# Performance work log

Hardware: AMD Instinct MI355X
Metric: run time of the kernel (lower is better)

## Reference

```python
import jax, jax.numpy as jnp
import numpy as np

D = 1024       # d_model
H = 16         # nhead
HD = D // H    # head_dim = 64
FF = 4096      # dim_feedforward
EPS = 1e-5


def layer_norm(x, gamma, beta, eps=EPS):
    mu = jnp.mean(x, axis=-1, keepdims=True)
    var = jnp.var(x, axis=-1, keepdims=True)
    return (x - mu) * jax.lax.rsqrt(var + eps) * gamma + beta


def setup_inputs() -> dict:
    key = jax.random.key(0)
    ks = jax.random.split(key, 12)
    rn = lambda k, shape, s=0.02: (jax.random.normal(k, shape, jnp.float32) * s)
    return {
        "src": jax.random.normal(ks[0], (4, 2048, D), jnp.float32),
        "Wqkv": rn(ks[1], (D, 3 * D)),          # qkv_proj weight (bias=False), stored (in,out)
        "Wout": rn(ks[2], (D, D)),              # out_proj weight (bias=False)
        "W1": rn(ks[3], (D, FF)),               # linear1
        "b1": jnp.zeros((FF,), jnp.float32),
        "W2": rn(ks[4], (FF, D)),               # linear2
        "b2": jnp.zeros((D,), jnp.float32),
        "g1": jnp.ones((D,), jnp.float32),      # norm1 weight
        "be1": jnp.zeros((D,), jnp.float32),    # norm1 bias
        "g2": jnp.ones((D,), jnp.float32),      # norm2 weight
        "be2": jnp.zeros((D,), jnp.float32),    # norm2 bias
    }


def reference(src, Wqkv, Wout, W1, b1, W2, b2, g1, be1, g2, be2):
    B, S, _ = src.shape
    # --- self attention (naive/MATH-backend SDPA, post-norm, eval: dropout=0) ---
    qkv = src @ Wqkv                                  # [B,S,3D]
    qkv = qkv.reshape(B, S, 3, H, HD)
    q = qkv[:, :, 0].transpose(0, 2, 1, 3)            # [B,H,S,HD]
    k = qkv[:, :, 1].transpose(0, 2, 1, 3)
    v = qkv[:, :, 2].transpose(0, 2, 1, 3)
    scores = jnp.einsum("bhqd,bhkd->bhqk", q, k) / np.float32(np.sqrt(HD))  # [B,H,S,S]
    attn = jax.nn.softmax(scores, axis=-1)
    ctx = jnp.einsum("bhqk,bhkd->bhqd", attn, v)      # [B,H,S,HD]
    ctx = ctx.transpose(0, 2, 1, 3).reshape(B, S, D)  # [B,S,D]
    attn_out = ctx @ Wout
    # residual + norm1
    x = layer_norm(src + attn_out, g1, be1)
    # --- FFN ---
    ff = jax.nn.relu(x @ W1 + b1) @ W2 + b2
    # residual + norm2
    return layer_norm(x + ff, g2, be2)
```

## Files before the change

kernel.cpp:

```cpp
#include <hip/hip_runtime.h>
#include <hip/hip_bf16.h>


typedef __attribute__((ext_vector_type(8))) short          short8;
typedef __attribute__((ext_vector_type(8))) unsigned short ushort8;
typedef __attribute__((ext_vector_type(4))) float          f32x4;
typedef __attribute__((ext_vector_type(2))) unsigned int   uivec2;

__device__ __forceinline__ unsigned short f2bf(float f) {
    union { float f; unsigned int u; } v; v.f = f;
    unsigned int u = v.u;
    unsigned int r = (u + 0x7fffu + ((u >> 16) & 1u)) >> 16;
    return (unsigned short)r;
}

__device__ __forceinline__ float bf2f(unsigned short u) {
    union { unsigned int u; float f; } v; v.u = ((unsigned int)u) << 16;
    return v.f;
}

__device__ __forceinline__ unsigned int pack_bf16_trunc(float lo, float hi) {
    union { float f; unsigned int u; } a, b; a.f = lo; b.f = hi;
    return __builtin_amdgcn_perm(b.u, a.u, 0x07060302u);
}

__device__ __forceinline__ void async_load16(const void* g, void* l) {
    __builtin_amdgcn_global_load_lds(
        (const __attribute__((address_space(1))) void*)(unsigned long long)g,
        (__attribute__((address_space(3))) void*)(unsigned long long)l,
        16, 0, 0);
}

__global__ __launch_bounds__(256) void cast_bf16_kernel(
    const float* __restrict__ x, unsigned short* __restrict__ y) {
    size_t i = ((size_t)blockIdx.x * 256 + threadIdx.x) * 4;
    float4 v = *(const float4*)(x + i);
    ushort4 o; o.x = f2bf(v.x); o.y = f2bf(v.y); o.z = f2bf(v.z); o.w = f2bf(v.w);
    *(ushort4*)(y + i) = o;
}

__global__ __launch_bounds__(256) void transpose_cast_kernel(
    const float* __restrict__ W, unsigned short* __restrict__ Wt, int K, int N) {
    __shared__ float tile[32][33];
    int n0 = blockIdx.x * 32, k0 = blockIdx.y * 32;
    int tx = threadIdx.x & 31, ty = threadIdx.x >> 5;
#pragma unroll
    for (int i = 0; i < 32; i += 8)
        tile[ty + i][tx] = W[(size_t)(k0 + ty + i) * N + n0 + tx];
    __syncthreads();
#pragma unroll
    for (int i = 0; i < 32; i += 8)
        Wt[(size_t)(n0 + ty + i) * K + k0 + tx] = f2bf(tile[tx][ty + i]);
}

template <int MODE>
__global__ __launch_bounds__(256) void gemm_bf16_kernel(
    const unsigned short* __restrict__ A, const unsigned short* __restrict__ Bt,
    int M, int N, int K, int Kstride,
    float* __restrict__ outF, unsigned short* __restrict__ outB,
    const float* __restrict__ bias,
    const float* __restrict__ resF, const unsigned short* __restrict__ resB,
    unsigned short* __restrict__ vtB) {
    __shared__ unsigned short As[2][128 * 32];
    __shared__ unsigned short Bs[2][128 * 32];

    const int t = threadIdx.x;
    const int m0 = blockIdx.x * 128, n0 = blockIdx.y * 128;
    const int koff = blockIdx.z * K;
    const int wid = t >> 6, lane = t & 63;
    const int wm = wid >> 1, wn = wid & 1;
    const int lr = lane & 15, quad = lane >> 4;

    const int srow = lane >> 2;
    const int sch  = ((lane & 3) ^ (srow & 3)) * 8;
    const unsigned short* Ag =
        A  + (size_t)(m0 + wid * 32 + srow) * Kstride + koff + sch;
    const unsigned short* Bg =
        Bt + (size_t)(n0 + wid * 32 + srow) * Kstride + koff + sch;
    const int wofs = (wid * 32) * 32;
    const size_t rstep = (size_t)16 * Kstride;

    const int axs = ((quad ^ (lr & 3))) * 8;
    f32x4 acc[4][4] = {};

    const int nK = K >> 5;
    async_load16(Ag,         &As[0][wofs]);
    async_load16(Ag + rstep, &As[0][wofs + 16 * 32]);
    async_load16(Bg,         &Bs[0][wofs]);
    async_load16(Bg + rstep, &Bs[0][wofs + 16 * 32]);

    for (int kt = 0; kt < nK; kt++) {
        const int cur = kt & 1, nxt = cur ^ 1;
        __syncthreads();
        if (kt + 1 < nK) {
            const int k1 = (kt + 1) * 32;
            async_load16(Ag + k1,         &As[nxt][wofs]);
            async_load16(Ag + k1 + rstep, &As[nxt][wofs + 16 * 32]);
            async_load16(Bg + k1,         &Bs[nxt][wofs]);
            async_load16(Bg + k1 + rstep, &Bs[nxt][wofs + 16 * 32]);
        }

        short8 af[4], bfr[4];
#pragma unroll
        for (int i = 0; i < 4; i++) {
            af[i]  = *(const short8*)&As[cur][(wm * 64 + i * 16 + lr) * 32 + axs];
            bfr[i] = *(const short8*)&Bs[cur][(wn * 64 + i * 16 + lr) * 32 + axs];
        }
#pragma unroll
        for (int mi = 0; mi < 4; mi++)
#pragma unroll
            for (int ni = 0; ni < 4; ni++)
                acc[mi][ni] = __builtin_amdgcn_mfma_f32_16x16x32_bf16(
                    af[mi], bfr[ni], acc[mi][ni], 0, 0, 0);
    }

#pragma unroll
    for (int mi = 0; mi < 4; mi++)
#pragma unroll
        for (int ni = 0; ni < 4; ni++) {
            const int col  = n0 + wn * 64 + ni * 16 + lr;
            const int row0 = m0 + wm * 64 + mi * 16 + quad * 4;
#pragma unroll
            for (int r = 0; r < 4; r++) {
                size_t idx = (size_t)(row0 + r) * N + col;
                float v = acc[mi][ni][r];
                if (MODE == 0) {
                    outB[idx] = f2bf(v);
                } else if (MODE == 1) {
                    outF[idx] = v + resF[idx];
                }
            }
        }
}

#define GBAR() do { __builtin_amdgcn_sched_barrier(0); \
                    __builtin_amdgcn_s_barrier();      \
                    __builtin_amdgcn_sched_barrier(0); } while (0)

template <int MODE>
__global__ __launch_bounds__(512, 2) void gemm256_bf16_kernel(
    const unsigned short* __restrict__ A, const unsigned short* __restrict__ Bt,
    int M, int N, int K, int Kstride,
    float* __restrict__ outF, unsigned short* __restrict__ outB,
    const float* __restrict__ bias,
    const float* __restrict__ resF, const unsigned short* __restrict__ resB,
    unsigned short* __restrict__ vtB) {
    __shared__ unsigned short Alds[4][256 * 32];
    __shared__ unsigned short Blds[4][256 * 32];

    const int t = threadIdx.x;
    const int wid = t >> 6, lane = t & 63;
    const int wm = wid >> 2, wn = wid & 3;
    const int lr = lane & 15, quad = lane >> 4;
    const int m0 = blockIdx.x * 256, n0 = blockIdx.y * 256;
    const int koff = blockIdx.z * K;

    const int srow = wid * 32 + (lane >> 2);
    const int sch  = ((lane & 3) ^ (srow & 3)) * 8;
    const unsigned short* Ag = A  + (size_t)(m0 + srow) * Kstride + koff + sch;
    const unsigned short* Bg = Bt + (size_t)(n0 + srow) * Kstride + koff + sch;
    const size_t rstep = (size_t)16 * Kstride;
    unsigned short* AdstW = &Alds[0][(wid * 32) * 32];
    unsigned short* BdstW = &Blds[0][(wid * 32) * 32];

    const int axs = (quad ^ (lr & 3)) * 8;

    f32x4 acc[8][4] = {};
    short8 bfr[4];

    const int T = K >> 6;
    const int Tm2 = T - 2, Tm3 = T - 3;

#define STAGE_A(GP) do { int s_ = (GP) & 3;                                   \
        const unsigned short* g_ = Ag + (GP) * 32;                            \
        async_load16(g_,         AdstW + s_ * 256 * 32);                      \
        async_load16(g_ + rstep, AdstW + s_ * 256 * 32 + 16 * 32); } while (0)
#define STAGE_B(GP) do { int s_ = (GP) & 3;                                   \
        const unsigned short* g_ = Bg + (GP) * 32;                            \
        async_load16(g_,         BdstW + s_ * 256 * 32);                      \
        async_load16(g_ + rstep, BdstW + s_ * 256 * 32 + 16 * 32); } while (0)

    STAGE_A(0); STAGE_B(0);
    STAGE_A(1); STAGE_B(1);
    STAGE_A(2); STAGE_B(2);
    asm volatile("s_waitcnt vmcnt(4)" ::: "memory");
    GBAR();

#define GPHASE(SLOT, MB, LOADB)                                               \
    {                                                                         \
        short8 af_[4];                                                        \
        _Pragma("unroll")                                                     \
        for (int i_ = 0; i_ < 4; i_++)                                        \
            af_[i_] = *(const short8*)                                        \
                &Alds[SLOT][(wm * 128 + ((MB) + i_) * 16 + lr) * 32 + axs];   \
        if (LOADB) {                                                          \
            _Pragma("unroll")                                                 \
            for (int i_ = 0; i_ < 4; i_++)                                    \
                bfr[i_] = *(const short8*)                                    \
                    &Blds[SLOT][(wn * 64 + i_ * 16 + lr) * 32 + axs];         \
        }

#define GPHASE_END(MB)                                                        \
        GBAR();                                                               \
        asm volatile("s_waitcnt lgkmcnt(0)" ::: "memory");                    \
        __builtin_amdgcn_sched_barrier(0);                                    \
        __builtin_amdgcn_s_setprio(1);                                        \
        _Pragma("unroll")                                                     \
        for (int mi_ = 0; mi_ < 4; mi_++)                                     \
            _Pragma("unroll")                                                 \
            for (int ni_ = 0; ni_ < 4; ni_++)                                 \
                acc[(MB) + mi_][ni_] = __builtin_amdgcn_mfma_f32_16x16x32_bf16( \
                    af_[mi_], bfr[ni_], acc[(MB) + mi_][ni_], 0, 0, 0);       \
        __builtin_amdgcn_s_setprio(0);                                        \
        GBAR();                                                               \
    }

    for (int t2 = 0; t2 < T; t2++) {
        const int s0 = (2 * t2) & 3, s1 = (2 * t2 + 1) & 3;
        const int gA = 2 * t2 + 3, gB = 2 * t2 + 4;

        GPHASE(s0, 0, 1)
            if (t2 <= Tm2) STAGE_A(gA);
        GPHASE_END(0)
        GPHASE(s0, 4, 0)
            if (t2 <= Tm2) STAGE_B(gA);
        GPHASE_END(4)
        GPHASE(s1, 0, 1)
            if (t2 <= Tm3) STAGE_A(gB);
        GPHASE_END(0)
        GPHASE(s1, 4, 0)
            if (t2 <= Tm3) STAGE_B(gB);
            if (t2 == Tm2) {
                asm volatile("s_waitcnt vmcnt(0)" ::: "memory");
            } else if (t2 < Tm2) {
                asm volatile("s_waitcnt vmcnt(4)" ::: "memory");
            }
        GPHASE_END(4)
    }

#undef GPHASE
#undef GPHASE_END
#undef STAGE_A
#undef STAGE_B

    const float QSC = 0.18033688011112042f;
    float* pOut = (MODE == 5) ? outF + (size_t)blockIdx.z * M * N : outF;
#pragma unroll
    for (int mi = 0; mi < 8; mi++)
#pragma unroll
        for (int ni = 0; ni < 4; ni++) {
            const int col  = n0 + wn * 64 + ni * 16 + lr;
            const int row0 = m0 + wm * 128 + mi * 16 + quad * 4;
            if (MODE == 4 && col >= 2048) {
                int bb = row0 >> 11, ss = row0 & 2047, c = col - 2048;
                ushort4 ov;
                ov.x = f2bf(acc[mi][ni][0]); ov.y = f2bf(acc[mi][ni][1]);
                ov.z = f2bf(acc[mi][ni][2]); ov.w = f2bf(acc[mi][ni][3]);
                *(ushort4*)&vtB[((size_t)bb * 1024 + c) * 2048 + ss] = ov;
            } else {
#pragma unroll
                for (int r = 0; r < 4; r++) {
                    size_t idx = (size_t)(row0 + r) * N + col;
                    float v = acc[mi][ni][r];
                    if (MODE == 4) {
                        outB[idx] = f2bf(col < 1024 ? v * QSC : v);
                    } else if (MODE == 2) {
                        v += bias[col];
                        outB[idx] = f2bf(v > 0.f ? v : 0.f);
                    } else if (MODE == 5) {
                        pOut[idx] = v;
                    }
                }
            }
        }
}

__global__ __launch_bounds__(256) void attention_kernel(
    const unsigned short* __restrict__ qkv, const unsigned short* __restrict__ Vt,
    unsigned short* __restrict__ ctx) {
    __shared__ unsigned short Kbuf[2][64 * 64];
    __shared__ unsigned short Vbuf[2][64 * 64];

    const int qt = blockIdx.x, h = blockIdx.y, b = blockIdx.z;
    const int t = threadIdx.x, wid = t >> 6, lane = t & 63;
    const int lr = lane & 15, quad = lane >> 4;
    const int q0 = qt * 64 + wid * 16;

    size_t qbase = ((size_t)(b * 2048 + q0 + lr)) * 3072 + h * 64;
    short8 qf0 = *(const short8*)(qkv + qbase + quad * 8);
    short8 qf1 = *(const short8*)(qkv + qbase + 32 + quad * 8);

    const int srow = wid * 8 + (lane >> 3);
    const int sch  = ((lane & 7) ^ (srow & 7)) * 8;
    const unsigned short* Kg =
        qkv + (size_t)b * 2048 * 3072 + 1024 + h * 64 + (size_t)srow * 3072 + sch;
    const unsigned short* Vg =
        Vt + ((size_t)b * 1024 + h * 64 + srow) * 2048 + sch;
    unsigned short* KsB = (unsigned short*)&Kbuf[0][(wid * 8) * 64];
    unsigned short* VsB = (unsigned short*)&Vbuf[0][(wid * 8) * 64];
    const int bufstep = 64 * 64;

    short8 ones;
#pragma unroll
    for (int i = 0; i < 8; i++) ones[i] = (short)0x3F80;

    f32x4 o[4] = {};
    f32x4 lacc = {};

#pragma unroll
    for (int half = 0; half < 2; half++) {
        async_load16(Kg + (size_t)(half * 32) * 3072, KsB + half * 32 * 64);
        async_load16(Vg + (size_t)(half * 32) * 2048, VsB + half * 32 * 64);
    }

    const int swz = lr & 7;

    for (int kt = 0; kt < 32; kt++) {
        const int cur = kt & 1, nxt = cur ^ 1;
        __syncthreads();
        if (kt + 1 < 32) {
#pragma unroll
            for (int half = 0; half < 2; half++) {
                async_load16(Kg + (size_t)((kt + 1) * 64 + half * 32) * 3072,
                             KsB + nxt * bufstep + half * 32 * 64);
                async_load16(Vg + (size_t)(half * 32) * 2048 + (kt + 1) * 64,
                             VsB + nxt * bufstep + half * 32 * 64);
            }
        }

        const unsigned short* Kc = &Kbuf[cur][0];
        const unsigned short* Vc = &Vbuf[cur][0];

        f32x4 s[4] = {};
#pragma unroll
        for (int nt = 0; nt < 4; nt++) {
            const unsigned short* krow = Kc + (nt * 16 + lr) * 64;
            short8 kf0 = *(const short8*)(krow + (quad ^ swz) * 8);
            short8 kf1 = *(const short8*)(krow + ((quad + 4) ^ swz) * 8);
            s[nt] = __builtin_amdgcn_mfma_f32_16x16x32_bf16(kf0, qf0, s[nt], 0, 0, 0);
            s[nt] = __builtin_amdgcn_mfma_f32_16x16x32_bf16(kf1, qf1, s[nt], 0, 0, 0);
        }

        unsigned int aw[4], bw[4];
#pragma unroll
        for (int nt = 0; nt < 4; nt++) {
            float p0 = __builtin_amdgcn_exp2f(s[nt][0]);
            float p1 = __builtin_amdgcn_exp2f(s[nt][1]);
            float p2 = __builtin_amdgcn_exp2f(s[nt][2]);
            float p3 = __builtin_amdgcn_exp2f(s[nt][3]);
            aw[nt] = pack_bf16_trunc(p0, p1);
            bw[nt] = pack_bf16_trunc(p2, p3);
        }

        uivec2 rA = __builtin_amdgcn_permlane32_swap(aw[0], aw[1], false, false);
        uivec2 sA = __builtin_amdgcn_permlane32_swap(aw[2], aw[3], false, false);
        uivec2 rB = __builtin_amdgcn_permlane32_swap(bw[0], bw[1], false, false);
        uivec2 sB = __builtin_amdgcn_permlane32_swap(bw[2], bw[3], false, false);
        uivec2 tA = __builtin_amdgcn_permlane16_swap(rA.x, rA.y, false, false);
        uivec2 uA = __builtin_amdgcn_permlane16_swap(sA.x, sA.y, false, false);
        uivec2 tB = __builtin_amdgcn_permlane16_swap(rB.x, rB.y, false, false);
        uivec2 uB = __builtin_amdgcn_permlane16_swap(sB.x, sB.y, false, false);

        union { unsigned int w[4]; short8 v; } P0, P1;
        P0.w[0] = tA.x; P0.w[1] = tB.x; P0.w[2] = tA.y; P0.w[3] = tB.y;
        P1.w[0] = uA.x; P1.w[1] = uB.x; P1.w[2] = uA.y; P1.w[3] = uB.y;
        short8 pf0 = P0.v;
        short8 pf1 = P1.v;

#pragma unroll
        for (int nt = 0; nt < 4; nt++) {
            const unsigned short* vrow = Vc + (nt * 16 + lr) * 64;
            short8 vf0 = *(const short8*)(vrow + (quad ^ swz) * 8);
            short8 vf1 = *(const short8*)(vrow + ((quad + 4) ^ swz) * 8);
            o[nt] = __builtin_amdgcn_mfma_f32_16x16x32_bf16(pf0, vf0, o[nt], 0, 0, 0);
            o[nt] = __builtin_amdgcn_mfma_f32_16x16x32_bf16(pf1, vf1, o[nt], 0, 0, 0);
        }
        lacc = __builtin_amdgcn_mfma_f32_16x16x32_bf16(pf0, ones, lacc, 0, 0, 0);
        lacc = __builtin_amdgcn_mfma_f32_16x16x32_bf16(pf1, ones, lacc, 0, 0, 0);
    }

#pragma unroll
    for (int r = 0; r < 4; r++) {
        float li = 1.f / lacc[r];
        int q = qt * 64 + wid * 16 + quad * 4 + r;
#pragma unroll
        for (int nt = 0; nt < 4; nt++)
            ctx[((size_t)(b * 2048 + q)) * 1024 + h * 64 + nt * 16 + lr] =
                f2bf(o[nt][r] * li);
    }
}

template <int OUTMODE>
__global__ __launch_bounds__(256) void layernorm_kernel(
    const float* __restrict__ x, const float* __restrict__ g,
    const float* __restrict__ be, float* __restrict__ yF,
    unsigned short* __restrict__ yB) {
    const int row = blockIdx.x, t = threadIdx.x;
    const float* xr = x + (size_t)row * 1024;
    float4 v = *(const float4*)(xr + t * 4);
    float s  = v.x + v.y + v.z + v.w;
    float sq = v.x * v.x + v.y * v.y + v.z * v.z + v.w * v.w;
#pragma unroll
    for (int d = 1; d < 64; d <<= 1) {
        s  += __shfl_xor(s, d, 64);
        sq += __shfl_xor(sq, d, 64);
    }
    __shared__ float sh[8];
    int wid = t >> 6, lane = t & 63;
    if (lane == 0) { sh[wid] = s; sh[4 + wid] = sq; }
    __syncthreads();
    s  = sh[0] + sh[1] + sh[2] + sh[3];
    sq = sh[4] + sh[5] + sh[6] + sh[7];
    float mu  = s * (1.f / 1024.f);
    float var = sq * (1.f / 1024.f) - mu * mu;
    float rstd = rsqrtf(var + 1e-5f);
    float4 gv = *(const float4*)(g + t * 4);
    float4 bv = *(const float4*)(be + t * 4);
    float4 y;
    y.x = (v.x - mu) * rstd * gv.x + bv.x;
    y.y = (v.y - mu) * rstd * gv.y + bv.y;
    y.z = (v.z - mu) * rstd * gv.z + bv.z;
    y.w = (v.w - mu) * rstd * gv.w + bv.w;
    if (OUTMODE == 0) {
        *(float4*)(yF + (size_t)row * 1024 + t * 4) = y;
    } else {
        ushort4 o;
        o.x = f2bf(y.x); o.y = f2bf(y.y); o.z = f2bf(y.z); o.w = f2bf(y.w);
        *(ushort4*)(yB + (size_t)row * 1024 + t * 4) = o;
    }
}

__global__ __launch_bounds__(256) void layernorm_sum2_kernel(
    const float* __restrict__ p0, const float* __restrict__ p1,
    const float* __restrict__ bias, const unsigned short* __restrict__ res,
    const float* __restrict__ g, const float* __restrict__ be,
    float* __restrict__ out) {
    const int row = blockIdx.x, t = threadIdx.x;
    const size_t base = (size_t)row * 1024 + t * 4;
    float4 a = *(const float4*)(p0 + base);
    float4 b = *(const float4*)(p1 + base);
    float4 bi = *(const float4*)(bias + t * 4);
    ushort4 rb = *(const ushort4*)(res + base);
    float4 v;
    v.x = a.x + b.x + bi.x + bf2f(rb.x);
    v.y = a.y + b.y + bi.y + bf2f(rb.y);
    v.z = a.z + b.z + bi.z + bf2f(rb.z);
    v.w = a.w + b.w + bi.w + bf2f(rb.w);
    float s  = v.x + v.y + v.z + v.w;
    float sq = v.x * v.x + v.y * v.y + v.z * v.z + v.w * v.w;
#pragma unroll
    for (int d = 1; d < 64; d <<= 1) {
        s  += __shfl_xor(s, d, 64);
        sq += __shfl_xor(sq, d, 64);
    }
    __shared__ float sh[8];
    int wid = t >> 6, lane = t & 63;
    if (lane == 0) { sh[wid] = s; sh[4 + wid] = sq; }
    __syncthreads();
    s  = sh[0] + sh[1] + sh[2] + sh[3];
    sq = sh[4] + sh[5] + sh[6] + sh[7];
    float mu  = s * (1.f / 1024.f);
    float var = sq * (1.f / 1024.f) - mu * mu;
    float rstd = rsqrtf(var + 1e-5f);
    float4 gv = *(const float4*)(g + t * 4);
    float4 bv = *(const float4*)(be + t * 4);
    float4 y;
    y.x = (v.x - mu) * rstd * gv.x + bv.x;
    y.y = (v.y - mu) * rstd * gv.y + bv.y;
    y.z = (v.z - mu) * rstd * gv.z + bv.z;
    y.w = (v.w - mu) * rstd * gv.w + bv.w;
    *(float4*)(out + base) = y;
}

extern "C" void kernel_launch(void* const* d_in, const int* in_sizes, int n_in,
                              void* d_out, int out_size, void* d_ws, size_t ws_size,
                              hipStream_t stream) {
    const float* src  = (const float*)d_in[0];
    const float* Wqkv = (const float*)d_in[1];
    const float* Wout = (const float*)d_in[2];
    const float* W1   = (const float*)d_in[3];
    const float* b1   = (const float*)d_in[4];
    const float* W2   = (const float*)d_in[5];
    const float* b2   = (const float*)d_in[6];
    const float* g1   = (const float*)d_in[7];
    const float* be1  = (const float*)d_in[8];
    const float* g2   = (const float*)d_in[9];
    const float* be2  = (const float*)d_in[10];
    float* out = (float*)d_out;

    const size_t NT = 8192;
    char* ws = (char*)d_ws;
    unsigned short* src_bf = (unsigned short*)ws; ws += NT * 1024 * 2;
    unsigned short* Wqkv_t = (unsigned short*)ws; ws += (size_t)3072 * 1024 * 2;
    unsigned short* Wout_t = (unsigned short*)ws; ws += (size_t)1024 * 1024 * 2;
    unsigned short* W1_t   = (unsigned short*)ws; ws += (size_t)4096 * 1024 * 2;
    unsigned short* W2_t   = (unsigned short*)ws; ws += (size_t)1024 * 4096 * 2;
    unsigned short* qkv_bf = (unsigned short*)ws; ws += NT * 3072 * 2;
    unsigned short* ctx_bf = (unsigned short*)ws; ws += NT * 1024 * 2;
    float*          x1     = (float*)ws;          ws += NT * 1024 * 4;
    unsigned short* y1_bf  = (unsigned short*)ws; ws += NT * 1024 * 2;
    unsigned short* h_bf   = (unsigned short*)ws; ws += NT * 4096 * 2;
    unsigned short* Vt = h_bf;
    float* part = (float*)qkv_bf;

    cast_bf16_kernel<<<8192, 256, 0, stream>>>(src, src_bf);
    transpose_cast_kernel<<<dim3(96, 32), 256, 0, stream>>>(Wqkv, Wqkv_t, 1024, 3072);
    transpose_cast_kernel<<<dim3(32, 32), 256, 0, stream>>>(Wout, Wout_t, 1024, 1024);
    transpose_cast_kernel<<<dim3(128, 32), 256, 0, stream>>>(W1, W1_t, 1024, 4096);
    transpose_cast_kernel<<<dim3(32, 128), 256, 0, stream>>>(W2, W2_t, 4096, 1024);

    gemm256_bf16_kernel<4><<<dim3(32, 12), 512, 0, stream>>>(
        src_bf, Wqkv_t, 8192, 3072, 1024, 1024,
        nullptr, qkv_bf, nullptr, nullptr, nullptr, Vt);
    attention_kernel<<<dim3(32, 16, 4), 256, 0, stream>>>(qkv_bf, Vt, ctx_bf);
    gemm_bf16_kernel<1><<<dim3(64, 8), 256, 0, stream>>>(
        ctx_bf, Wout_t, 8192, 1024, 1024, 1024,
        x1, nullptr, nullptr, src, nullptr, nullptr);
    layernorm_kernel<1><<<8192, 256, 0, stream>>>(x1, g1, be1, nullptr, y1_bf);
    gemm256_bf16_kernel<2><<<dim3(32, 16), 512, 0, stream>>>(
        y1_bf, W1_t, 8192, 4096, 1024, 1024,
        nullptr, h_bf, b1, nullptr, nullptr, nullptr);
    gemm256_bf16_kernel<5><<<dim3(32, 4, 2), 512, 0, stream>>>(
        h_bf, W2_t, 8192, 1024, 2048, 4096,
        part, nullptr, nullptr, nullptr, nullptr, nullptr);
    layernorm_sum2_kernel<<<8192, 256, 0, stream>>>(
        part, part + NT * 1024, b2, y1_bf, g2, be2, out);
}
```

Measured before the change: 543.3 us.

## Restructure 256x256 GEMM pipeline to double-buffered 64-wide K tiles with XCD remap

Replaces the 4-slot 32-wide K staging with two 64-wide K tile buffers, where a whole tile is loaded ahead and waited on once per 64-K step instead of per half-phase. The LDS swizzle changes to an 8-chunk XOR pattern to match the wider rows. It also remaps workgroup IDs so consecutive blocks are grouped by chiplet, to improve L2 locality. The trade-off is coarser overlap: all loads for the next tile are issued only after compute, and sched_barrier fences around the barriers are dropped. That could let the compiler reorder LDS accesses across barriers, and the ID remap assumes the workgroup count is divisible by 8.

```diff
diff --git a/kernel.cpp b/kernel.cpp
--- a/kernel.cpp
+++ b/kernel.cpp
@@ -133,10 +133,6 @@
         }
 }
 
-#define GBAR() do { __builtin_amdgcn_sched_barrier(0); \
-                    __builtin_amdgcn_s_barrier();      \
-                    __builtin_amdgcn_sched_barrier(0); } while (0)
-
 template <int MODE>
 __global__ __launch_bounds__(512, 2) void gemm256_bf16_kernel(
     const unsigned short* __restrict__ A, const unsigned short* __restrict__ Bt,
@@ -145,63 +141,57 @@
     const float* __restrict__ bias,
     const float* __restrict__ resF, const unsigned short* __restrict__ resB,
     unsigned short* __restrict__ vtB) {
-    __shared__ unsigned short Alds[4][256 * 32];
-    __shared__ unsigned short Blds[4][256 * 32];
+    __shared__ unsigned short Ald[2][256 * 64];
+    __shared__ unsigned short Bld[2][256 * 64];
 
     const int t = threadIdx.x;
     const int wid = t >> 6, lane = t & 63;
     const int wm = wid >> 2, wn = wid & 3;
     const int lr = lane & 15, quad = lane >> 4;
-    const int m0 = blockIdx.x * 256, n0 = blockIdx.y * 256;
+
+    const int gx = gridDim.x, nwg = gx * gridDim.y;
+    const int id = blockIdx.y * gx + blockIdx.x;
+    const int nid = (id & 7) * (nwg >> 3) + (id >> 3);
+    const int m0 = (nid % gx) * 256, n0 = (nid / gx) * 256;
     const int koff = blockIdx.z * K;
 
-    const int srow = wid * 32 + (lane >> 2);
-    const int sch  = ((lane & 3) ^ (srow & 3)) * 8;
+    const int srow = wid * 32 + (lane >> 3);
+    const int sch  = ((lane & 7) ^ (lane >> 3)) * 8;
     const unsigned short* Ag = A  + (size_t)(m0 + srow) * Kstride + koff + sch;
     const unsigned short* Bg = Bt + (size_t)(n0 + srow) * Kstride + koff + sch;
-    const size_t rstep = (size_t)16 * Kstride;
-    unsigned short* AdstW = &Alds[0][(wid * 32) * 32];
-    unsigned short* BdstW = &Blds[0][(wid * 32) * 32];
-
-    const int axs = (quad ^ (lr & 3)) * 8;
+    const size_t rstep8 = (size_t)8 * Kstride;
+    unsigned short* Abase = &Ald[0][(wid * 32) * 64];
+    unsigned short* Bbase = &Bld[0][(wid * 32) * 64];
 
     f32x4 acc[8][4] = {};
     short8 bfr[4];
-
     const int T = K >> 6;
-    const int Tm2 = T - 2, Tm3 = T - 3;
-
-#define STAGE_A(GP) do { int s_ = (GP) & 3;                                   \
-        const unsigned short* g_ = Ag + (GP) * 32;                            \
-        async_load16(g_,         AdstW + s_ * 256 * 32);                      \
-        async_load16(g_ + rstep, AdstW + s_ * 256 * 32 + 16 * 32); } while (0)
-#define STAGE_B(GP) do { int s_ = (GP) & 3;                                   \
-        const unsigned short* g_ = Bg + (GP) * 32;                            \
-        async_load16(g_,         BdstW + s_ * 256 * 32);                      \
-        async_load16(g_ + rstep, BdstW + s_ * 256 * 32 + 16 * 32); } while (0)
-
-    STAGE_A(0); STAGE_B(0);
-    STAGE_A(1); STAGE_B(1);
-    STAGE_A(2); STAGE_B(2);
-    asm volatile("s_waitcnt vmcnt(4)" ::: "memory");
-    GBAR();
-
-#define GPHASE(SLOT, MB, LOADB)                                               \
+
+#define STAGE_TILE(TT) do { const int b_ = (TT) & 1; const int c_ = (TT) * 64; \
+        _Pragma("unroll")                                                      \
+        for (int i_ = 0; i_ < 4; i_++) {                                       \
+            async_load16(Ag + c_ + i_ * rstep8,                                \
+                         Abase + b_ * 256 * 64 + i_ * 8 * 64);                 \
+            async_load16(Bg + c_ + i_ * rstep8,                                \
+                         Bbase + b_ * 256 * 64 + i_ * 8 * 64);                 \
+        } } while (0)
+
+#define PH(KH, MB, LOADB)                                                     \
     {                                                                         \
         short8 af_[4];                                                        \
         _Pragma("unroll")                                                     \
         for (int i_ = 0; i_ < 4; i_++)                                        \
-            af_[i_] = *(const short8*)                                        \
-                &Alds[SLOT][(wm * 128 + ((MB) + i_) * 16 + lr) * 32 + axs];   \
+            af_[i_] = *(const short8*)&Ald[cb][                               \
+                (wm * 128 + ((MB) + i_) * 16 + lr) * 64 +                     \
+                (((quad + (KH) * 4)) ^ (lr & 7)) * 8];                        \
         if (LOADB) {                                                          \
             _Pragma("unroll")                                                 \
             for (int i_ = 0; i_ < 4; i_++)                                    \
-                bfr[i_] = *(const short8*)                                    \
-                    &Blds[SLOT][(wn * 64 + i_ * 16 + lr) * 32 + axs];         \
-        }
-
-#define GPHASE_END(MB)                                                        \
-        GBAR();                                                               \
+                bfr[i_] = *(const short8*)&Bld[cb][                           \
+                    (wn * 64 + i_ * 16 + lr) * 64 +                           \
+                    (((quad + (KH) * 4)) ^ (lr & 7)) * 8];                    \
+        }                                                                     \
+        __builtin_amdgcn_s_barrier();                                         \
         asm volatile("s_waitcnt lgkmcnt(0)" ::: "memory");                    \
         __builtin_amdgcn_sched_barrier(0);                                    \
         __builtin_amdgcn_s_setprio(1);                                        \
@@ -212,36 +202,31 @@
                 acc[(MB) + mi_][ni_] = __builtin_amdgcn_mfma_f32_16x16x32_bf16( \
                     af_[mi_], bfr[ni_], acc[(MB) + mi_][ni_], 0, 0, 0);       \
         __builtin_amdgcn_s_setprio(0);                                        \
-        GBAR();                                                               \
-    }
-
-    for (int t2 = 0; t2 < T; t2++) {
-        const int s0 = (2 * t2) & 3, s1 = (2 * t2 + 1) & 3;
-        const int gA = 2 * t2 + 3, gB = 2 * t2 + 4;
-
-        GPHASE(s0, 0, 1)
-            if (t2 <= Tm2) STAGE_A(gA);
-        GPHASE_END(0)
-        GPHASE(s0, 4, 0)
-            if (t2 <= Tm2) STAGE_B(gA);
-        GPHASE_END(4)
-        GPHASE(s1, 0, 1)
-            if (t2 <= Tm3) STAGE_A(gB);
-        GPHASE_END(0)
-        GPHASE(s1, 4, 0)
-            if (t2 <= Tm3) STAGE_B(gB);
-            if (t2 == Tm2) {
-                asm volatile("s_waitcnt vmcnt(0)" ::: "memory");
-            } else if (t2 < Tm2) {
-                asm volatile("s_waitcnt vmcnt(4)" ::: "memory");
-            }
-        GPHASE_END(4)
-    }
-
-#undef GPHASE
-#undef GPHASE_END
-#undef STAGE_A
-#undef STAGE_B
+        __builtin_amdgcn_s_barrier();                                         \
+    }
+
+    STAGE_TILE(0);
+    STAGE_TILE(1);
+
+    for (int kt = 0; kt < T; kt++) {
+        const int cb = kt & 1;
+        if (kt < T - 1) {
+            asm volatile("s_waitcnt vmcnt(8)" ::: "memory");
+        } else {
+            asm volatile("s_waitcnt vmcnt(0)" ::: "memory");
+        }
+        __builtin_amdgcn_s_barrier();
+
+        PH(0, 0, 1)
+        PH(0, 4, 0)
+        PH(1, 0, 1)
+        PH(1, 4, 0)
+
+        if (kt + 2 < T) STAGE_TILE(kt + 2);
+    }
+
+#undef PH
+#undef STAGE_TILE
 
     const float QSC = 0.18033688011112042f;
     float* pOut = (MODE == 5) ? outF + (size_t)blockIdx.z * M * N : outF;
```

Result: no change. 542.8 us (-0.1%).
